# Optimization experiments

Hardware: AMD Instinct MI355X
Metric: run time of the kernel (lower is better)

Reference implementation:

```python
import jax, jax.numpy as jnp
import numpy as np

B, T, I, H, O = 64, 128, 512, 1024, 512

def setup_inputs() -> dict:
    key = jax.random.key(0)
    ks = jax.random.split(key, 4)
    std = 1.0 / np.sqrt(H)
    xs = jax.random.normal(ks[0], (B, T, I), dtype=jnp.float32)
    # fused gate weights: order (i, f, g, o)
    W_ih = jax.random.uniform(ks[1], (I, 4 * H), minval=-std, maxval=std, dtype=jnp.float32)
    W_hh = jax.random.uniform(ks[2], (H, 4 * H), minval=-std, maxval=std, dtype=jnp.float32)
    b = jnp.zeros((4 * H,), dtype=jnp.float32)
    W_o = jax.random.uniform(ks[3], (H, O), minval=-std, maxval=std, dtype=jnp.float32)
    b_o = jnp.zeros((O,), dtype=jnp.float32)
    return {"xs": xs, "W_ih": W_ih, "W_hh": W_hh, "b": b, "W_o": W_o, "b_o": b_o}

def reference(xs, W_ih, W_hh, b, W_o, b_o):
    act = jax.nn.relu  # activation='relu' replaces tanh in the cell
    # precompute input contribution for all timesteps: [B, T, 4H]
    x_gates = jnp.einsum('bti,ig->btg', xs, W_ih) + b

    def step(carry, xg):
        h, c = carry
        gates = xg + h @ W_hh  # [B, 4H]
        i, f, g, o = jnp.split(gates, 4, axis=-1)
        i = jax.nn.sigmoid(i)
        f = jax.nn.sigmoid(f)
        g = act(g)
        o = jax.nn.sigmoid(o)
        c = f * c + i * g
        h = o * act(c)
        return (h, c), None

    h0 = jnp.zeros((xs.shape[0], W_hh.shape[0]), dtype=xs.dtype)
    c0 = jnp.zeros_like(h0)
    (h_t, _), _ = jax.lax.scan(step, (h0, c0), jnp.swapaxes(x_gates, 0, 1))
    return h_t @ W_o + b_o  # [B, O]
```

## Files before the change

### kernel.cpp

```cpp
#include <hip/hip_runtime.h>

typedef unsigned int uint;
typedef unsigned short ushort;
typedef __attribute__((ext_vector_type(8))) short short8;
typedef __attribute__((ext_vector_type(16))) float f32x16;
typedef __attribute__((ext_vector_type(4))) uint uintx4;

#define T_STEPS 128
#define NGRP 128
#define NCNT 8
#define CPW 8

__device__ __forceinline__ ushort f2bf(float f) {
  union { float f; uint u; } v; v.f = f;
  uint r = v.u + 0x7fffu + ((v.u >> 16) & 1u);
  return (ushort)(r >> 16);
}
__device__ __forceinline__ float bf2f(ushort u) {
  union { uint u; float f; } v; v.u = ((uint)u) << 16;
  return v.f;
}

union F8 { uint4 u4; short8 s; };


__global__ void convert_xs_kernel(const float* __restrict__ xs, ushort* __restrict__ xb) {
  int idx = blockIdx.x * 256 + threadIdx.x;
  int t = idx >> 12;
  int b = (idx >> 6) & 63;
  int j = idx & 63;
  const float* src = xs + (b * 128 + t) * 512 + j * 8;
  float4 a = *(const float4*)src;
  float4 c = *(const float4*)(src + 4);
  union { ushort r[8]; uint4 v; } p;
  p.r[0] = f2bf(a.x); p.r[1] = f2bf(a.y); p.r[2] = f2bf(a.z); p.r[3] = f2bf(a.w);
  p.r[4] = f2bf(c.x); p.r[5] = f2bf(c.y); p.r[6] = f2bf(c.z); p.r[7] = f2bf(c.w);
  *(uint4*)(xb + t * 32768 + j * 512 + b * 8) = p.v;
}

__global__ void transpose_w_kernel(const float* __restrict__ W, ushort* __restrict__ WT, int ko) {
  __shared__ ushort tile[32][33];
  int kt = blockIdx.x * 32, nt = blockIdx.y * 32;
  int tx = threadIdx.x & 31, ty = threadIdx.x >> 5;
#pragma unroll
  for (int i = 0; i < 4; ++i) {
    int kk = ty + i * 8;
    tile[kk][tx] = f2bf(W[(kt + kk) * 4096 + nt + tx]);
  }
  __syncthreads();
#pragma unroll
  for (int i = 0; i < 4; ++i) {
    int nn = ty + i * 8;
    WT[(nt + nn) * 1536 + ko + kt + tx] = tile[tx][nn];
  }
}


__global__ __launch_bounds__(512, 1) void lstm_persist(
    const ushort* __restrict__ xsb, const ushort* __restrict__ WT,
    const float* __restrict__ bias, const float* __restrict__ Wo,
    const float* __restrict__ bo, ushort* __restrict__ hbuf,
    uint* __restrict__ cnt, float* __restrict__ out) {

  __shared__ float sP[8 * 2 * 16 * 64];
  __shared__ ushort tr[512];

  const int tid = threadIdx.x;
  const int wg  = blockIdx.x;
  const int lane = tid & 63;
  const int wv = tid >> 6;
  const int c  = lane & 31;
  const int hi = lane >> 5;
  const int rep = wg >> 6;
  const int wgu = wg & 63;

  const int gc0 = ((c >> 4)) * 1024 + wgu * 16 + (c & 15);
  const int gc1 = (2 + (c >> 4)) * 1024 + wgu * 16 + (c & 15);
  uint4 Wx[4][2], Wh[8][2];
#pragma unroll
  for (int kf = 0; kf < 4; ++kf) {
    int k = wv * 64 + kf * 16 + hi * 8;
    Wx[kf][0] = *(const uint4*)(WT + gc0 * 1536 + k);
    Wx[kf][1] = *(const uint4*)(WT + gc1 * 1536 + k);
  }
#pragma unroll
  for (int i = 0; i < 8; ++i) {
    int k = 512 + (wv * 8 + i) * 16 + hi * 8;
    Wh[i][0] = *(const uint4*)(WT + gc0 * 1536 + k);
    Wh[i][1] = *(const uint4*)(WT + gc1 * 1536 + k);
  }

  const float bc0 = bias[gc0];
  const float bc1 = bias[gc1];
  const int r0f = wv * 2;
  float cst[2] = {0.f, 0.f};

  for (int t = 0; t < T_STEPS; ++t) {
    const ushort* __restrict__ hrd = hbuf + t * 65536 + rep * 32768;
    ushort* __restrict__ hwr = hbuf + (t + 1) * 65536 + rep * 32768;

    uint4 Ax[4];
    {
      const ushort* xst = xsb + t * 32768 + rep * 256 + c * 8;
#pragma unroll
      for (int kf = 0; kf < 4; ++kf)
        Ax[kf] = *(const uint4*)(xst + (wv * 8 + kf * 2 + hi) * 512);
    }

    if (t > 0) {
      if (wv == 0 && lane < NCNT) {
        uint tgt = (uint)(CPW * t);
        while (__hip_atomic_load(cnt + (rep * 8 + lane) * 32, __ATOMIC_RELAXED,
                                 __HIP_MEMORY_SCOPE_AGENT) < tgt)
          __builtin_amdgcn_s_sleep(2);
      }
      __syncthreads();
    }

    uint4 Ah[8];
    {
      const ushort* hb = hrd + (wv * 8) * 512 + c * 16 + hi * 8;
#pragma unroll
      for (int i = 0; i < 8; ++i)
        Ah[i] = *(const uint4*)(hb + i * 512);
    }

    f32x16 acc0 = {}, acc1 = {};
#pragma unroll
    for (int kf = 0; kf < 4; ++kf) {
      F8 a, w0, w1; a.u4 = Ax[kf]; w0.u4 = Wx[kf][0]; w1.u4 = Wx[kf][1];
      acc0 = __builtin_amdgcn_mfma_f32_32x32x16_bf16(a.s, w0.s, acc0, 0, 0, 0);
      acc1 = __builtin_amdgcn_mfma_f32_32x32x16_bf16(a.s, w1.s, acc1, 0, 0, 0);
    }
#pragma unroll
    for (int i = 0; i < 8; ++i) {
      F8 a, w0, w1; a.u4 = Ah[i]; w0.u4 = Wh[i][0]; w1.u4 = Wh[i][1];
      acc0 = __builtin_amdgcn_mfma_f32_32x32x16_bf16(a.s, w0.s, acc0, 0, 0, 0);
      acc1 = __builtin_amdgcn_mfma_f32_32x32x16_bf16(a.s, w1.s, acc1, 0, 0, 0);
    }

    {
      float* p = sP + wv * 2048 + lane;
#pragma unroll
      for (int r = 0; r < 16; ++r) p[r * 64] = acc0[r];
#pragma unroll
      for (int r = 0; r < 16; ++r) p[1024 + r * 64] = acc1[r];
    }
    __syncthreads();

#pragma unroll
    for (int s = 0; s < 2; ++s) {
      int r = r0f + s;
      int o = r * 64 + lane;
      float f0 = bc0, f1 = bc1;
#pragma unroll
      for (int w = 0; w < 8; ++w) {
        f0 += sP[w * 2048 + o];
        f1 += sP[w * 2048 + 1024 + o];
      }
      float ff = __shfl_xor(f0, 16);
      float oo = __shfl_xor(f1, 16);
      float ig = 1.f / (1.f + __expf(-f0));
      float fg = 1.f / (1.f + __expf(-ff));
      float gg = fmaxf(f1, 0.f);
      float og = 1.f / (1.f + __expf(-oo));
      float cn = fg * cst[s] + ig * gg;
      cst[s] = cn;
      ushort hv = f2bf(og * fmaxf(cn, 0.f));
      if (c < 16) {
        int row = (r & 3) + 8 * (r >> 2) + 4 * hi;
        tr[row * 16 + c] = hv;
      }
    }
    __syncthreads();

    if (wv == 0) {
      uintx4 hq = *(const uintx4*)((const ushort*)tr + lane * 8);
      asm volatile("global_store_dwordx4 %0, %1, off sc1"
                   :: "v"(hwr + wgu * 512 + lane * 8), "v"(hq) : "memory");
      asm volatile("s_waitcnt vmcnt(0)" ::: "memory");
      if (lane == 0)
        __hip_atomic_fetch_add(cnt + (rep * 8 + (wgu & 7)) * 32, 1u,
                               __ATOMIC_RELAXED, __HIP_MEMORY_SCOPE_AGENT);
    }
  }

  if (wv == 0 && lane < 16) {
    uint tgt = (uint)(CPW * T_STEPS);
    while (__hip_atomic_load(cnt + lane * 32, __ATOMIC_RELAXED,
                             __HIP_MEMORY_SCOPE_AGENT) < tgt)
      __builtin_amdgcn_s_sleep(2);
  }
  __syncthreads();
  if (tid < 256) {
    int oidx = wg * 256 + tid;
    int b = oidx >> 9, oc = oidx & 511;
    int rep2 = b >> 5, row = b & 31;
    const ushort* hf = hbuf + T_STEPS * 65536 + rep2 * 32768 + row * 16;
    float s = bo[oc];
#pragma unroll 2
    for (int w = 0; w < 64; ++w) {
      uint4 h0 = *(const uint4*)(hf + w * 512);
      uint4 h1 = *(const uint4*)(hf + w * 512 + 8);
      const ushort* p0 = (const ushort*)&h0;
      const ushort* p1 = (const ushort*)&h1;
#pragma unroll
      for (int j = 0; j < 8; ++j)
        s = fmaf(bf2f(p0[j]), Wo[(w * 16 + j) * 512 + oc], s);
#pragma unroll
      for (int j = 0; j < 8; ++j)
        s = fmaf(bf2f(p1[j]), Wo[(w * 16 + 8 + j) * 512 + oc], s);
    }
    out[oidx] = s;
  }
}


extern "C" void kernel_launch(void* const* d_in, const int* in_sizes, int n_in,
                              void* d_out, int out_size, void* d_ws, size_t ws_size,
                              hipStream_t stream) {
  (void)in_sizes; (void)n_in; (void)out_size; (void)ws_size;
  const float* xs  = (const float*)d_in[0];
  const float* Wih = (const float*)d_in[1];
  const float* Whh = (const float*)d_in[2];
  const float* b   = (const float*)d_in[3];
  const float* Wo  = (const float*)d_in[4];
  const float* bo  = (const float*)d_in[5];
  float* out = (float*)d_out;

  char* ws = (char*)d_ws;
  uint* cnt    = (uint*)ws;
  ushort* hbuf = (ushort*)(ws + 4096);
  ushort* xsb  = (ushort*)(ws + 4096 + 16908288);
  ushort* WT   = (ushort*)(ws + 4096 + 16908288 + 8388608);

  hipMemsetAsync(ws, 0, 4096 + 131072, stream);
  convert_xs_kernel<<<2048, 256, 0, stream>>>(xs, xsb);
  transpose_w_kernel<<<dim3(16, 128), 256, 0, stream>>>(Wih, WT, 0);
  transpose_w_kernel<<<dim3(32, 128), 256, 0, stream>>>(Whh, WT, 512);
  lstm_persist<<<NGRP, 512, 0, stream>>>(xsb, WT, b, Wo, bo, hbuf, cnt, out);
}
```

Baseline: 480.3 us.

## Replace counter barrier with per-workgroup step flags and overlap x-projection MFMAs

Replaces the shared atomic counters with one flag per workgroup that holds the last completed step. Each wave polls only the eight producer flags whose h slices it reads, so there is no block-wide barrier before the h loads. The input-projection MFMAs now run before the wait, overlapping the x contribution with the cross-workgroup synchronization latency. Hidden outputs are written directly to global memory as scattered short stores instead of being staged through LDS for one vectorized store, which trades fewer barriers for more, smaller store transactions.

```diff
diff --git a/kernel.cpp b/kernel.cpp
--- a/kernel.cpp
+++ b/kernel.cpp
@@ -4,12 +4,9 @@
 typedef unsigned short ushort;
 typedef __attribute__((ext_vector_type(8))) short short8;
 typedef __attribute__((ext_vector_type(16))) float f32x16;
-typedef __attribute__((ext_vector_type(4))) uint uintx4;
 
 #define T_STEPS 128
 #define NGRP 128
-#define NCNT 8
-#define CPW 8
 
 __device__ __forceinline__ ushort f2bf(float f) {
   union { float f; uint u; } v; v.f = f;
@@ -60,10 +57,9 @@
     const ushort* __restrict__ xsb, const ushort* __restrict__ WT,
     const float* __restrict__ bias, const float* __restrict__ Wo,
     const float* __restrict__ bo, ushort* __restrict__ hbuf,
-    uint* __restrict__ cnt, float* __restrict__ out) {
+    uint* __restrict__ flg, float* __restrict__ out) {
 
   __shared__ float sP[8 * 2 * 16 * 64];
-  __shared__ ushort tr[512];
 
   const int tid = threadIdx.x;
   const int wg  = blockIdx.x;
@@ -106,31 +102,30 @@
       for (int kf = 0; kf < 4; ++kf)
         Ax[kf] = *(const uint4*)(xst + (wv * 8 + kf * 2 + hi) * 512);
     }
-
-    if (t > 0) {
-      if (wv == 0 && lane < NCNT) {
-        uint tgt = (uint)(CPW * t);
-        while (__hip_atomic_load(cnt + (rep * 8 + lane) * 32, __ATOMIC_RELAXED,
-                                 __HIP_MEMORY_SCOPE_AGENT) < tgt)
-          __builtin_amdgcn_s_sleep(2);
-      }
-      __syncthreads();
-    }
-
-    uint4 Ah[8];
-    {
-      const ushort* hb = hrd + (wv * 8) * 512 + c * 16 + hi * 8;
-#pragma unroll
-      for (int i = 0; i < 8; ++i)
-        Ah[i] = *(const uint4*)(hb + i * 512);
-    }
-
     f32x16 acc0 = {}, acc1 = {};
 #pragma unroll
     for (int kf = 0; kf < 4; ++kf) {
       F8 a, w0, w1; a.u4 = Ax[kf]; w0.u4 = Wx[kf][0]; w1.u4 = Wx[kf][1];
       acc0 = __builtin_amdgcn_mfma_f32_32x32x16_bf16(a.s, w0.s, acc0, 0, 0, 0);
       acc1 = __builtin_amdgcn_mfma_f32_32x32x16_bf16(a.s, w1.s, acc1, 0, 0, 0);
+    }
+
+    if (t > 0) {
+      if (lane < 8) {
+        const uint tgt = (uint)t;
+        const uint* fp = flg + (rep * 64 + wv * 8 + lane) * 32;
+        while (__hip_atomic_load(fp, __ATOMIC_RELAXED, __HIP_MEMORY_SCOPE_AGENT) < tgt)
+          __builtin_amdgcn_s_sleep(1);
+      }
+      asm volatile("" ::: "memory");
+    }
+
+    uint4 Ah[8];
+    {
+      const ushort* hb = hrd + (wv * 8) * 512 + c * 16 + hi * 8;
+#pragma unroll
+      for (int i = 0; i < 8; ++i)
+        Ah[i] = *(const uint4*)(hb + i * 512);
     }
 #pragma unroll
     for (int i = 0; i < 8; ++i) {
@@ -169,26 +164,21 @@
       ushort hv = f2bf(og * fmaxf(cn, 0.f));
       if (c < 16) {
         int row = (r & 3) + 8 * (r >> 2) + 4 * hi;
-        tr[row * 16 + c] = hv;
+        asm volatile("global_store_short %0, %1, off sc1"
+                     :: "v"(hwr + wgu * 512 + row * 16 + c), "v"((uint)hv) : "memory");
       }
     }
+    asm volatile("s_waitcnt vmcnt(0)" ::: "memory");
     __syncthreads();
 
-    if (wv == 0) {
-      uintx4 hq = *(const uintx4*)((const ushort*)tr + lane * 8);
-      asm volatile("global_store_dwordx4 %0, %1, off sc1"
-                   :: "v"(hwr + wgu * 512 + lane * 8), "v"(hq) : "memory");
-      asm volatile("s_waitcnt vmcnt(0)" ::: "memory");
-      if (lane == 0)
-        __hip_atomic_fetch_add(cnt + (rep * 8 + (wgu & 7)) * 32, 1u,
-                               __ATOMIC_RELAXED, __HIP_MEMORY_SCOPE_AGENT);
-    }
-  }
-
-  if (wv == 0 && lane < 16) {
-    uint tgt = (uint)(CPW * T_STEPS);
-    while (__hip_atomic_load(cnt + lane * 32, __ATOMIC_RELAXED,
-                             __HIP_MEMORY_SCOPE_AGENT) < tgt)
+    if (tid == 0)
+      __hip_atomic_store(flg + (rep * 64 + wgu) * 32, (uint)(t + 1),
+                         __ATOMIC_RELAXED, __HIP_MEMORY_SCOPE_AGENT);
+  }
+
+  if (tid < 64) {
+    const uint* fp = flg + (rep * 64 + tid) * 32;
+    while (__hip_atomic_load(fp, __ATOMIC_RELAXED, __HIP_MEMORY_SCOPE_AGENT) < (uint)T_STEPS)
       __builtin_amdgcn_s_sleep(2);
   }
   __syncthreads();
@@ -229,14 +219,14 @@
   float* out = (float*)d_out;
 
   char* ws = (char*)d_ws;
-  uint* cnt    = (uint*)ws;
-  ushort* hbuf = (ushort*)(ws + 4096);
-  ushort* xsb  = (ushort*)(ws + 4096 + 16908288);
-  ushort* WT   = (ushort*)(ws + 4096 + 16908288 + 8388608);
-
-  hipMemsetAsync(ws, 0, 4096 + 131072, stream);
+  uint* flg    = (uint*)ws;
+  ushort* hbuf = (ushort*)(ws + 16384);
+  ushort* xsb  = (ushort*)(ws + 16384 + 16908288);
+  ushort* WT   = (ushort*)(ws + 16384 + 16908288 + 8388608);
+
+  hipMemsetAsync(ws, 0, 16384 + 131072, stream);
   convert_xs_kernel<<<2048, 256, 0, stream>>>(xs, xsb);
   transpose_w_kernel<<<dim3(16, 128), 256, 0, stream>>>(Wih, WT, 0);
   transpose_w_kernel<<<dim3(32, 128), 256, 0, stream>>>(Whh, WT, 512);
-  lstm_persist<<<NGRP, 512, 0, stream>>>(xsb, WT, b, Wo, bo, hbuf, cnt, out);
-}
+  lstm_persist<<<NGRP, 512, 0, stream>>>(xsb, WT, b, Wo, bo, hbuf, flg, out);
+}
```

Result: slower. 508.7 us (+5.9%).
